# Kernel tuning notes

Hardware: AMD Instinct MI355X
Metric: run time of the kernel (lower is better)

## Reference

```python
import jax, jax.numpy as jnp
import numpy as np

B, P = 4, 65536
TD, HID, OUT = 32, 128, 4
RES = 256
NFREQ = 6
CD = 3 * 2 * NFREQ  # frequency encoding out dim


def setup_inputs() -> dict:
    key = jax.random.key(0)
    ks = jax.random.split(key, 12)

    def w(k, shape):
        fan_in = shape[-1]
        return jax.random.normal(k, shape, jnp.float32) / np.sqrt(fan_in)

    return {
        "triplane": jax.random.normal(ks[0], (3 * B, TD, RES, RES), jnp.float32),
        "coords": jax.random.uniform(ks[1], (B, P, 3), jnp.float32),  # inside aabb [-1,1]^3
        "w_in": w(ks[2], (HID, TD + CD)),
        "b_in": jnp.zeros((HID,), jnp.float32),
        "w_skip": w(ks[3], (HID, TD + CD)),
        "b_skip": jnp.zeros((HID,), jnp.float32),
        "w_before": w(ks[4], (2, HID, HID)),
        "b_before": jnp.zeros((2, HID), jnp.float32),
        "w_after": w(ks[5], (2, HID, HID)),
        "b_after": jnp.zeros((2, HID), jnp.float32),
        "w_out": w(ks[6], (OUT, HID)),
        "b_out": jnp.zeros((OUT,), jnp.float32),
    }


@jax.custom_vjp
def trunc_exp(x):
    return jnp.exp(x)


def _trunc_exp_fwd(x):
    return jnp.exp(x), x


def _trunc_exp_bwd(x, g):
    return (g * jnp.exp(jnp.clip(x, -15.0, 15.0)),)


trunc_exp.defvjp(_trunc_exp_fwd, _trunc_exp_bwd)


def grid_sample_bilinear(feat, gx, gy):
    # feat: [N, C, H, W]; gx, gy: [N, Q] in [-1, 1]; align_corners=True, zero padding.
    N, C, H, W = feat.shape
    ix = (gx + 1.0) * 0.5 * (W - 1)
    iy = (gy + 1.0) * 0.5 * (H - 1)
    x0 = jnp.floor(ix)
    y0 = jnp.floor(iy)
    wx1 = ix - x0
    wy1 = iy - y0
    feat_flat = feat.reshape(N, C, H * W)

    def gather(xf, yf):
        xi = xf.astype(jnp.int32)
        yi = yf.astype(jnp.int32)
        valid = ((xi >= 0) & (xi < W) & (yi >= 0) & (yi < H)).astype(feat.dtype)
        xi = jnp.clip(xi, 0, W - 1)
        yi = jnp.clip(yi, 0, H - 1)
        idx = yi * W + xi  # [N, Q]
        g = jnp.take_along_axis(feat_flat, idx[:, None, :], axis=2)  # [N, C, Q]
        return g * valid[:, None, :]

    out = (
        gather(x0, y0) * ((1 - wx1) * (1 - wy1))[:, None, :]
        + gather(x0 + 1, y0) * (wx1 * (1 - wy1))[:, None, :]
        + gather(x0, y0 + 1) * ((1 - wx1) * wy1)[:, None, :]
        + gather(x0 + 1, y0 + 1) * (wx1 * wy1)[:, None, :]
    )
    return out  # [N, C, Q]


def freq_encode(x):
    # x: [B, P, 3] in [0, 1]; NeRF-style frequency encoding (tcnn 'Frequency').
    freqs = (2.0 ** jnp.arange(NFREQ, dtype=x.dtype)) * jnp.pi  # [NFREQ]
    ang = x[..., :, None] * freqs  # [B, P, 3, NFREQ]
    enc = jnp.concatenate([jnp.sin(ang), jnp.cos(ang)], axis=-1)  # [B, P, 3, 2*NFREQ]
    return enc.reshape(x.shape[0], x.shape[1], CD)


def reference(triplane, coords, w_in, b_in, w_skip, b_skip, w_before, b_before,
              w_after, b_after, w_out, b_out):
    aabb_min = jnp.full((3,), -1.0, jnp.float32)
    aabb_max = jnp.full((3,), 1.0, jnp.float32)

    scaled = 2.0 * (coords - aabb_min) / (aabb_max - aabb_min) - 1.0  # [-1,1]
    norm = (coords - aabb_min) / (aabb_max - aabb_min)  # [0,1]
    selector = jnp.all((norm > 0.0) & (norm < 1.0), axis=-1)  # [B, P]

    # planes: xy=(x,y), xz=(x,z), zy=(y,z); stacked per batch -> [3B, P, 2]
    coords_xy = scaled[:, :, (0, 1)]
    coords_xz = scaled[:, :, (0, 2)]
    coords_zy = scaled[:, :, (1, 2)]
    grid = jnp.stack([coords_xy, coords_xz, coords_zy], axis=1).reshape(3 * B, P, 2)

    feats = grid_sample_bilinear(triplane, grid[..., 0], grid[..., 1])  # [3B, TD, P]
    feats = feats.transpose(0, 2, 1).reshape(B, 3, P, TD).sum(axis=1)  # [B, P, TD]

    h = jnp.concatenate([freq_encode(norm), feats], axis=-1)  # [B, P, CD+TD]

    lin = lambda x, w, b: jnp.einsum("bpf,hf->bph", x, w) + b
    x = jax.nn.relu(lin(h, w_in, b_in))
    for i in range(w_before.shape[0]):
        x = jax.nn.relu(lin(x, w_before[i], b_before[i]))
    x = x + jax.nn.relu(lin(h, w_skip, b_skip))
    for i in range(w_after.shape[0]):
        x = jax.nn.relu(lin(x, w_after[i], b_after[i]))
    x = lin(x, w_out, b_out)  # [B, P, 4]

    rgb = jax.nn.sigmoid(x[..., :3])
    density = trunc_exp(x[..., 3:4] - 1.0) * selector[..., None].astype(x.dtype)
    return rgb, density
```

## Files before the change

kernel.cpp:

```cpp
#include <hip/hip_runtime.h>
#include <stdint.h>

typedef short short8 __attribute__((ext_vector_type(8)));
typedef float floatx16 __attribute__((ext_vector_type(16)));
typedef unsigned int uint32;

#define NPTS (4 * 65536)
#define RGB_OFF (NPTS * 3)

__device__ __forceinline__ uint16_t bf_rne(float f) {
  uint32 u = __float_as_uint(f);
  u += 0x7FFFu + ((u >> 16) & 1u);
  return (uint16_t)(u >> 16);
}
__device__ __forceinline__ uint32 pack2(float a, float b) {
  uint32 ua = (__float_as_uint(a) + 0x8000u) >> 16;
  uint32 ub = (__float_as_uint(b) + 0x8000u) & 0xFFFF0000u;
  return ua | ub;
}
__device__ __forceinline__ void gacc(const uint16_t* p, float w, float* acc) {
  uint4 q = *(const uint4*)p;
  acc[0] += w * __uint_as_float(q.x << 16);
  acc[1] += w * __uint_as_float(q.x & 0xFFFF0000u);
  acc[2] += w * __uint_as_float(q.y << 16);
  acc[3] += w * __uint_as_float(q.y & 0xFFFF0000u);
  acc[4] += w * __uint_as_float(q.z << 16);
  acc[5] += w * __uint_as_float(q.z & 0xFFFF0000u);
  acc[6] += w * __uint_as_float(q.w << 16);
  acc[7] += w * __uint_as_float(q.w & 0xFFFF0000u);
}

__global__ __launch_bounds__(256) void k_tr(const float* __restrict__ tri,
                                            uint16_t* __restrict__ out) {
  __shared__ uint16_t tile[32 * 258];
  const int blk = blockIdx.x;
  const int n = blk >> 8, y = blk & 255;
  const int t = threadIdx.x;
  for (int c = 0; c < 32; ++c) {
    float v = tri[((size_t)(n * 32 + c)) * 65536 + y * 256 + t];
    tile[c * 258 + t] = bf_rne(v);
  }
  __syncthreads();
  uint16_t* dst = out + ((size_t)(n * 256 + y)) * 256 * 32;
  const int c0 = (t & 7) * 4;
  for (int i = 0; i < 8; ++i) {
    int x = (t >> 3) + 32 * i;
    uint32 d0 = (uint32)tile[(c0 + 0) * 258 + x] | ((uint32)tile[(c0 + 1) * 258 + x] << 16);
    uint32 d1 = (uint32)tile[(c0 + 2) * 258 + x] | ((uint32)tile[(c0 + 3) * 258 + x] << 16);
    *(uint2*)(dst + x * 32 + c0) = make_uint2(d0, d1);
  }
}

__global__ __launch_bounds__(256) void k_pack(
    const float* __restrict__ w_in, const float* __restrict__ w_skip,
    const float* __restrict__ w_before, const float* __restrict__ w_after,
    const float* __restrict__ w_out, const float* __restrict__ b_in,
    const float* __restrict__ b_skip, const float* __restrict__ b_before,
    const float* __restrict__ b_after, const float* __restrict__ b_out,
    uint16_t* __restrict__ wpack, float* __restrict__ bpack) {
  const int blk = blockIdx.x;
  if (blk >= 44) {
    for (int t = threadIdx.x; t < 800; t += 256) {
      int l, idx;
      if (t < 768) { l = t >> 7; idx = t & 127; }
      else { l = 6; idx = t - 768; }
      int mt = idx >> 5, rem = idx & 31;
      int half = rem >> 4, r = rem & 15;
      int f = mt * 32 + (r & 3) + 8 * (r >> 2) + 4 * half;
      float v;
      switch (l) {
        case 0: v = b_in[f]; break;
        case 1: v = b_before[f]; break;
        case 2: v = b_before[128 + f]; break;
        case 3: v = b_skip[f]; break;
        case 4: v = b_after[f]; break;
        case 5: v = b_after[128 + f]; break;
        default: v = (f < 4) ? b_out[f] : 0.0f; break;
      }
      bpack[l * 128 + idx] = v;
    }
    return;
  }
  const int w = blk * 4 + (threadIdx.x >> 6);
  const int L = threadIdx.x & 63;
  int lay, mt, k;
  if (w < 20)      { lay = 0; mt = w / 5;        k = w - mt * 5; }
  else if (w < 52) { int u = w - 20;  lay = 1; mt = u >> 3; k = u & 7; }
  else if (w < 84) { int u = w - 52;  lay = 2; mt = u >> 3; k = u & 7; }
  else if (w < 104){ int u = w - 84;  lay = 3; mt = u / 5;  k = u - mt * 5; }
  else if (w < 136){ int u = w - 104; lay = 4; mt = u >> 3; k = u & 7; }
  else if (w < 168){ int u = w - 136; lay = 5; mt = u >> 3; k = u & 7; }
  else             { lay = 6; mt = 0; k = w - 168; }
  const float* W;
  int insk = 0;
  switch (lay) {
    case 0: W = w_in; insk = 1; break;
    case 1: W = w_before; break;
    case 2: W = w_before + 16384; break;
    case 3: W = w_skip; insk = 1; break;
    case 4: W = w_after; break;
    case 5: W = w_after + 16384; break;
    default: W = w_out; break;
  }
  const int frow = mt * 32 + (L & 31);
  const int kbase = k * 16 + (L >> 5) * 8;
  uint16_t h[8];
#pragma unroll
  for (int j = 0; j < 8; ++j) {
    int kl = kbase + j;
    float v;
    if (insk) {
      int col = (kl < 32) ? (36 + kl) : ((kl < 68) ? (kl - 32) : -1);
      v = (col < 0) ? 0.0f : W[frow * 68 + col];
    } else if (lay == 6) {
      v = (frow < 4) ? W[frow * 128 + kl] : 0.0f;
    } else {
      v = W[frow * 128 + kl];
    }
    h[j] = bf_rne(v);
  }
  uint4 q;
  q.x = (uint32)h[0] | ((uint32)h[1] << 16);
  q.y = (uint32)h[2] | ((uint32)h[3] << 16);
  q.z = (uint32)h[4] | ((uint32)h[5] << 16);
  q.w = (uint32)h[6] | ((uint32)h[7] << 16);
  *(uint4*)(wpack + (size_t)w * 512 + L * 8) = q;
}

template <int LAY, int Ks, int FOFF, bool FROMH, bool SKIP>
__device__ __forceinline__ void mlp_layer(const uint16_t* __restrict__ hrow,
                                          uint16_t* __restrict__ arow,
                                          const uint16_t* __restrict__ wpack,
                                          const float* __restrict__ bpack,
                                          int ih, int kh, int L, int ps) {
  const uint16_t* src = FROMH ? hrow : (const uint16_t*)arow;
  short8 bfr[Ks];
#pragma unroll
  for (int k = 0; k < Ks; ++k)
    bfr[k] = *(const short8*)(src + (((2 * k + kh) ^ ps) << 3));
  if (!FROMH) __syncthreads();
#pragma unroll
  for (int m = 0; m < 2; ++m) {
    const int mt = ih * 2 + m;
    const float4* bp = (const float4*)(bpack + LAY * 128 + mt * 32 + kh * 16);
    float4 b0 = bp[0], b1 = bp[1], b2 = bp[2], b3 = bp[3];
    floatx16 acc;
    acc[0] = b0.x; acc[1] = b0.y; acc[2] = b0.z; acc[3] = b0.w;
    acc[4] = b1.x; acc[5] = b1.y; acc[6] = b1.z; acc[7] = b1.w;
    acc[8] = b2.x; acc[9] = b2.y; acc[10] = b2.z; acc[11] = b2.w;
    acc[12] = b3.x; acc[13] = b3.y; acc[14] = b3.z; acc[15] = b3.w;
    const uint16_t* wp = wpack + (size_t)(FOFF + mt * Ks) * 512 + L * 8;
#pragma unroll
    for (int k = 0; k < Ks; ++k) {
      short8 af = *(const short8*)(wp + k * 512);
      acc = __builtin_amdgcn_mfma_f32_32x32x16_bf16(af, bfr[k], acc, 0, 0, 0);
    }
#pragma unroll
    for (int g = 0; g < 4; ++g) {
      float v0 = fmaxf(acc[4 * g + 0], 0.f), v1 = fmaxf(acc[4 * g + 1], 0.f);
      float v2 = fmaxf(acc[4 * g + 2], 0.f), v3 = fmaxf(acc[4 * g + 3], 0.f);
      const int byte = 64 * mt + 16 * g + 8 * kh;
      uint16_t* dst =
          (uint16_t*)((char*)arow + ((((byte >> 4)) ^ ps) << 4) + (byte & 15));
      if (SKIP) {
        uint2 old = *(const uint2*)dst;
        v0 += __uint_as_float(old.x << 16);
        v1 += __uint_as_float(old.x & 0xFFFF0000u);
        v2 += __uint_as_float(old.y << 16);
        v3 += __uint_as_float(old.y & 0xFFFF0000u);
      }
      *(uint2*)dst = make_uint2(pack2(v0, v1), pack2(v2, v3));
    }
  }
  __syncthreads();
}

__global__ __launch_bounds__(256, 2) void k_main(
    const uint16_t* __restrict__ trit, const float* __restrict__ trif,
    const float* __restrict__ coords, const uint16_t* __restrict__ wpack,
    const float* __restrict__ bpack, float* __restrict__ dout, int fast) {
  __shared__ __align__(16) uint16_t h_s[64 * 128];
  __shared__ __align__(16) uint16_t a_s[64 * 128];
  const int t = threadIdx.x;

  {
    const int p = t >> 2, c = t & 3;
    const int pg = blockIdx.x * 64 + p;
    float cx = coords[pg * 3 + 0], cy = coords[pg * 3 + 1], cz = coords[pg * 3 + 2];
    float f1x = cx + 1.0f, f1y = cy + 1.0f, f1z = cz + 1.0f;
    float nx = f1x * 0.5f, ny = f1y * 0.5f, nz = f1z * 0.5f;
    float sx = f1x - 1.0f, sy = f1y - 1.0f, sz = f1z - 1.0f;
    bool sel = (nx > 0.f) & (nx < 1.f) & (ny > 0.f) & (ny < 1.f) & (nz > 0.f) & (nz < 1.f);
    const int b = pg >> 16;
    float acc[8];
#pragma unroll
    for (int j = 0; j < 8; ++j) acc[j] = 0.f;
#pragma unroll
    for (int pl = 0; pl < 3; ++pl) {
      float gx = (pl == 2) ? sy : sx;
      float gy = (pl == 0) ? sy : sz;
      float ix = ((gx + 1.0f) * 0.5f) * 255.0f;
      float iy = ((gy + 1.0f) * 0.5f) * 255.0f;
      float x0f = floorf(ix), y0f = floorf(iy);
      float wx = ix - x0f, wy = iy - y0f;
      float vx0 = (x0f >= 0.0f && x0f < 256.0f) ? 1.f : 0.f;
      float vx1 = (x0f >= -1.0f && x0f < 255.0f) ? 1.f : 0.f;
      float vy0 = (y0f >= 0.0f && y0f < 256.0f) ? 1.f : 0.f;
      float vy1 = (y0f >= -1.0f && y0f < 255.0f) ? 1.f : 0.f;
      int x0 = min(max((int)x0f, 0), 255), x1 = min(max((int)x0f + 1, 0), 255);
      int y0 = min(max((int)y0f, 0), 255), y1 = min(max((int)y0f + 1, 0), 255);
      float w00 = (1.f - wx) * (1.f - wy) * vx0 * vy0;
      float w10 = wx * (1.f - wy) * vx1 * vy0;
      float w01 = (1.f - wx) * wy * vx0 * vy1;
      float w11 = wx * wy * vx1 * vy1;
      const int n = 3 * b + pl;
      if (fast) {
        const uint16_t* base = trit + ((size_t)n << 21) + (c << 3);
        gacc(base + ((size_t)(y0 * 256 + x0) << 5), w00, acc);
        gacc(base + ((size_t)(y0 * 256 + x1) << 5), w10, acc);
        gacc(base + ((size_t)(y1 * 256 + x0) << 5), w01, acc);
        gacc(base + ((size_t)(y1 * 256 + x1) << 5), w11, acc);
      } else {
        const float* basef = trif + ((size_t)(n * 32 + c * 8) << 16);
#pragma unroll
        for (int jj = 0; jj < 8; ++jj) {
          const float* chp = basef + ((size_t)jj << 16);
          acc[jj] += w00 * chp[y0 * 256 + x0] + w10 * chp[y0 * 256 + x1] +
                     w01 * chp[y1 * 256 + x0] + w11 * chp[y1 * 256 + x1];
        }
      }
    }
    const int s = p & 15;
    uint16_t* hrow = h_s + p * 128;
    *(uint4*)(hrow + (((c ^ s)) << 3)) =
        make_uint4(pack2(acc[0], acc[1]), pack2(acc[2], acc[3]),
                   pack2(acc[4], acc[5]), pack2(acc[6], acc[7]));
    if (c < 3) {
      float nd = (c == 0) ? nx : (c == 1) ? ny : nz;
      float vals[12];
#pragma unroll
      for (int k = 0; k < 6; ++k) {
        float rev = nd * (0.5f * (float)(1 << k));
        float r = rev - rintf(rev);
        vals[k] = __builtin_amdgcn_sinf(r);
        vals[6 + k] = __builtin_amdgcn_cosf(r);
      }
#pragma unroll
      for (int iw = 0; iw < 3; ++iw) {
        int byte = 64 + 24 * c + 8 * iw;
        int chunk = byte >> 4, off = byte & 15;
        *(uint2*)((char*)hrow + (((chunk ^ s)) << 4) + off) =
            make_uint2(pack2(vals[4 * iw + 0], vals[4 * iw + 1]),
                       pack2(vals[4 * iw + 2], vals[4 * iw + 3]));
      }
    } else {
      *(uint2*)((char*)hrow + (((8 ^ s)) << 4) + 8) = make_uint2(0u, 0u);
      uint32 selw = sel ? 0x3F800000u : 0u;
      *(uint4*)((char*)hrow + (((9 ^ s)) << 4)) = make_uint4(0u, 0u, 0u, selw);
    }
  }
  __syncthreads();

  const int w = t >> 6, L = t & 63;
  const int ih = w & 1, jh = w >> 1;
  const int kh = L >> 5;
  const int prow = jh * 32 + (L & 31);
  const int ps = prow & 15;
  const uint16_t* hrow = h_s + prow * 128;
  uint16_t* arow = a_s + prow * 128;

  mlp_layer<0, 5, 0,   true,  false>(hrow, arow, wpack, bpack, ih, kh, L, ps);
  mlp_layer<1, 8, 20,  false, false>(hrow, arow, wpack, bpack, ih, kh, L, ps);
  mlp_layer<2, 8, 52,  false, false>(hrow, arow, wpack, bpack, ih, kh, L, ps);
  mlp_layer<3, 5, 84,  true,  true >(hrow, arow, wpack, bpack, ih, kh, L, ps);
  mlp_layer<4, 8, 104, false, false>(hrow, arow, wpack, bpack, ih, kh, L, ps);
  mlp_layer<5, 8, 136, false, false>(hrow, arow, wpack, bpack, ih, kh, L, ps);

  if (ih == 0) {
    short8 bfr[8];
#pragma unroll
    for (int k = 0; k < 8; ++k)
      bfr[k] = *(const short8*)(arow + (((2 * k + kh) ^ ps) << 3));
    const float4* bp = (const float4*)(bpack + 768 + kh * 16);
    float4 b0 = bp[0], b1 = bp[1], b2 = bp[2], b3 = bp[3];
    floatx16 acc;
    acc[0] = b0.x; acc[1] = b0.y; acc[2] = b0.z; acc[3] = b0.w;
    acc[4] = b1.x; acc[5] = b1.y; acc[6] = b1.z; acc[7] = b1.w;
    acc[8] = b2.x; acc[9] = b2.y; acc[10] = b2.z; acc[11] = b2.w;
    acc[12] = b3.x; acc[13] = b3.y; acc[14] = b3.z; acc[15] = b3.w;
    const uint16_t* wp = wpack + (size_t)168 * 512 + L * 8;
#pragma unroll
    for (int k = 0; k < 8; ++k) {
      short8 af = *(const short8*)(wp + k * 512);
      acc = __builtin_amdgcn_mfma_f32_32x32x16_bf16(af, bfr[k], acc, 0, 0, 0);
    }
    if (kh == 0) {
      const int pg = blockIdx.x * 64 + prow;
      const float l2e = 1.44269504f;
      float r0 = 1.0f / (1.0f + exp2f(-l2e * acc[0]));
      float r1 = 1.0f / (1.0f + exp2f(-l2e * acc[1]));
      float r2 = 1.0f / (1.0f + exp2f(-l2e * acc[2]));
      uint16_t sv = hrow[(((9 ^ ps)) << 3) + 7];
      float dens = exp2f((acc[3] - 1.0f) * l2e) * (sv ? 1.0f : 0.0f);
      dout[pg * 3 + 0] = r0;
      dout[pg * 3 + 1] = r1;
      dout[pg * 3 + 2] = r2;
      dout[RGB_OFF + pg] = dens;
    }
  }
}

extern "C" void kernel_launch(void* const* d_in, const int* in_sizes, int n_in,
                              void* d_out, int out_size, void* d_ws, size_t ws_size,
                              hipStream_t stream) {
  const float* tri = (const float*)d_in[0];
  const float* coords = (const float*)d_in[1];
  const float* w_in = (const float*)d_in[2];
  const float* b_in = (const float*)d_in[3];
  const float* w_skip = (const float*)d_in[4];
  const float* b_skip = (const float*)d_in[5];
  const float* w_bef = (const float*)d_in[6];
  const float* b_bef = (const float*)d_in[7];
  const float* w_aft = (const float*)d_in[8];
  const float* b_aft = (const float*)d_in[9];
  const float* w_out = (const float*)d_in[10];
  const float* b_out = (const float*)d_in[11];
  const size_t TRI_B = (size_t)12 * 256 * 256 * 32 * 2;
  const size_t WP_B = (size_t)176 * 1024;
  const size_t BP_B = 3200;
  char* ws = (char*)d_ws;
  const int fast = (ws_size >= TRI_B + WP_B + BP_B) ? 1 : 0;
  uint16_t* trit;
  uint16_t* wpk;
  float* bpk;
  if (fast) {
    trit = (uint16_t*)ws;
    wpk = (uint16_t*)(ws + TRI_B);
    bpk = (float*)(ws + TRI_B + WP_B);
  } else {
    trit = (uint16_t*)ws;
    wpk = (uint16_t*)ws;
    bpk = (float*)(ws + WP_B);
  }
  if (fast) k_tr<<<dim3(3072), dim3(256), 0, stream>>>(tri, trit);
  k_pack<<<dim3(45), dim3(256), 0, stream>>>(w_in, w_skip, w_bef, w_aft, w_out,
                                             b_in, b_skip, b_bef, b_aft, b_out,
                                             wpk, bpk);
  k_main<<<dim3(4096), dim3(256), 0, stream>>>(trit, tri, coords, wpk, bpk,
                                               (float*)d_out, fast);
}
```

Measured before the change: 295.2 us.

## Process 128 points per block with 2x2 MFMA register tiling per wave

Each block now handles 128 points instead of 64, and each wave computes a 2x2 tile of 32x32 MFMA outputs, so every weight fragment loaded from global memory feeds two point tiles and is fetched half as often per point. The gather phase gives each thread two 16-byte chunks of features and reorganizes the frequency-encoding writes as full 16-byte stores. pack2 now uses a single byte-permute instruction. The grid is halved and shared memory doubles to 64KB per block, which together with higher register use may reduce occupancy below the two blocks per CU requested.

```diff
diff --git a/kernel.cpp b/kernel.cpp
--- a/kernel.cpp
+++ b/kernel.cpp
@@ -14,9 +14,8 @@
   return (uint16_t)(u >> 16);
 }
 __device__ __forceinline__ uint32 pack2(float a, float b) {
-  uint32 ua = (__float_as_uint(a) + 0x8000u) >> 16;
-  uint32 ub = (__float_as_uint(b) + 0x8000u) & 0xFFFF0000u;
-  return ua | ub;
+  return __builtin_amdgcn_perm(__float_as_uint(b) + 0x8000u,
+                               __float_as_uint(a) + 0x8000u, 0x07060302u);
 }
 __device__ __forceinline__ void gacc(const uint16_t* p, float w, float* acc) {
   uint4 q = *(const uint4*)p;
@@ -128,48 +127,66 @@
 }
 
 template <int LAY, int Ks, int FOFF, bool FROMH, bool SKIP>
-__device__ __forceinline__ void mlp_layer(const uint16_t* __restrict__ hrow,
-                                          uint16_t* __restrict__ arow,
-                                          const uint16_t* __restrict__ wpack,
-                                          const float* __restrict__ bpack,
-                                          int ih, int kh, int L, int ps) {
-  const uint16_t* src = FROMH ? hrow : (const uint16_t*)arow;
-  short8 bfr[Ks];
-#pragma unroll
-  for (int k = 0; k < Ks; ++k)
-    bfr[k] = *(const short8*)(src + (((2 * k + kh) ^ ps) << 3));
+__device__ __forceinline__ void mlp_layer(
+    const uint16_t* __restrict__ hrow0, const uint16_t* __restrict__ hrow1,
+    uint16_t* __restrict__ arow0, uint16_t* __restrict__ arow1,
+    const uint16_t* __restrict__ wpack, const float* __restrict__ bpack,
+    int mt0, int kh, int L, int ps) {
+  const uint16_t* src0 = FROMH ? hrow0 : (const uint16_t*)arow0;
+  const uint16_t* src1 = FROMH ? hrow1 : (const uint16_t*)arow1;
+  short8 b0[Ks], b1[Ks];
+#pragma unroll
+  for (int k = 0; k < Ks; ++k) {
+    b0[k] = *(const short8*)(src0 + (((2 * k + kh) ^ ps) << 3));
+    b1[k] = *(const short8*)(src1 + (((2 * k + kh) ^ ps) << 3));
+  }
   if (!FROMH) __syncthreads();
-#pragma unroll
-  for (int m = 0; m < 2; ++m) {
-    const int mt = ih * 2 + m;
-    const float4* bp = (const float4*)(bpack + LAY * 128 + mt * 32 + kh * 16);
-    float4 b0 = bp[0], b1 = bp[1], b2 = bp[2], b3 = bp[3];
-    floatx16 acc;
-    acc[0] = b0.x; acc[1] = b0.y; acc[2] = b0.z; acc[3] = b0.w;
-    acc[4] = b1.x; acc[5] = b1.y; acc[6] = b1.z; acc[7] = b1.w;
-    acc[8] = b2.x; acc[9] = b2.y; acc[10] = b2.z; acc[11] = b2.w;
-    acc[12] = b3.x; acc[13] = b3.y; acc[14] = b3.z; acc[15] = b3.w;
-    const uint16_t* wp = wpack + (size_t)(FOFF + mt * Ks) * 512 + L * 8;
-#pragma unroll
-    for (int k = 0; k < Ks; ++k) {
-      short8 af = *(const short8*)(wp + k * 512);
-      acc = __builtin_amdgcn_mfma_f32_32x32x16_bf16(af, bfr[k], acc, 0, 0, 0);
-    }
+  floatx16 a00, a01, a10, a11;
+  {
+    const float4* bp0 = (const float4*)(bpack + LAY * 128 + mt0 * 32 + kh * 16);
+    const float4* bp1 = (const float4*)(bpack + LAY * 128 + (mt0 + 1) * 32 + kh * 16);
 #pragma unroll
     for (int g = 0; g < 4; ++g) {
-      float v0 = fmaxf(acc[4 * g + 0], 0.f), v1 = fmaxf(acc[4 * g + 1], 0.f);
-      float v2 = fmaxf(acc[4 * g + 2], 0.f), v3 = fmaxf(acc[4 * g + 3], 0.f);
-      const int byte = 64 * mt + 16 * g + 8 * kh;
-      uint16_t* dst =
-          (uint16_t*)((char*)arow + ((((byte >> 4)) ^ ps) << 4) + (byte & 15));
-      if (SKIP) {
-        uint2 old = *(const uint2*)dst;
-        v0 += __uint_as_float(old.x << 16);
-        v1 += __uint_as_float(old.x & 0xFFFF0000u);
-        v2 += __uint_as_float(old.y << 16);
-        v3 += __uint_as_float(old.y & 0xFFFF0000u);
-      }
-      *(uint2*)dst = make_uint2(pack2(v0, v1), pack2(v2, v3));
+      float4 v0 = bp0[g], v1 = bp1[g];
+      a00[4 * g + 0] = v0.x; a00[4 * g + 1] = v0.y; a00[4 * g + 2] = v0.z; a00[4 * g + 3] = v0.w;
+      a10[4 * g + 0] = v1.x; a10[4 * g + 1] = v1.y; a10[4 * g + 2] = v1.z; a10[4 * g + 3] = v1.w;
+    }
+    a01 = a00; a11 = a10;
+  }
+  const uint16_t* wp0 = wpack + (size_t)(FOFF + mt0 * Ks) * 512 + L * 8;
+  const uint16_t* wp1 = wp0 + (size_t)Ks * 512;
+#pragma unroll
+  for (int k = 0; k < Ks; ++k) {
+    short8 af0 = *(const short8*)(wp0 + k * 512);
+    short8 af1 = *(const short8*)(wp1 + k * 512);
+    a00 = __builtin_amdgcn_mfma_f32_32x32x16_bf16(af0, b0[k], a00, 0, 0, 0);
+    a01 = __builtin_amdgcn_mfma_f32_32x32x16_bf16(af0, b1[k], a01, 0, 0, 0);
+    a10 = __builtin_amdgcn_mfma_f32_32x32x16_bf16(af1, b0[k], a10, 0, 0, 0);
+    a11 = __builtin_amdgcn_mfma_f32_32x32x16_bf16(af1, b1[k], a11, 0, 0, 0);
+  }
+#pragma unroll
+  for (int mi = 0; mi < 2; ++mi) {
+    const int mt = mt0 + mi;
+#pragma unroll
+    for (int j = 0; j < 2; ++j) {
+      uint16_t* arow = j ? arow1 : arow0;
+      const floatx16& ac = mi ? (j ? a11 : a10) : (j ? a01 : a00);
+#pragma unroll
+      for (int g = 0; g < 4; ++g) {
+        float v0 = fmaxf(ac[4 * g + 0], 0.f), v1 = fmaxf(ac[4 * g + 1], 0.f);
+        float v2 = fmaxf(ac[4 * g + 2], 0.f), v3 = fmaxf(ac[4 * g + 3], 0.f);
+        const int byte = 64 * mt + 16 * g + 8 * kh;
+        uint16_t* dst =
+            (uint16_t*)((char*)arow + ((((byte >> 4)) ^ ps) << 4) + (byte & 15));
+        if (SKIP) {
+          uint2 old = *(const uint2*)dst;
+          v0 += __uint_as_float(old.x << 16);
+          v1 += __uint_as_float(old.x & 0xFFFF0000u);
+          v2 += __uint_as_float(old.y << 16);
+          v3 += __uint_as_float(old.y & 0xFFFF0000u);
+        }
+        *(uint2*)dst = make_uint2(pack2(v0, v1), pack2(v2, v3));
+      }
     }
   }
   __syncthreads();
@@ -179,22 +196,22 @@
     const uint16_t* __restrict__ trit, const float* __restrict__ trif,
     const float* __restrict__ coords, const uint16_t* __restrict__ wpack,
     const float* __restrict__ bpack, float* __restrict__ dout, int fast) {
-  __shared__ __align__(16) uint16_t h_s[64 * 128];
-  __shared__ __align__(16) uint16_t a_s[64 * 128];
+  __shared__ __align__(16) uint16_t h_s[128 * 128];
+  __shared__ __align__(16) uint16_t a_s[128 * 128];
   const int t = threadIdx.x;
 
   {
-    const int p = t >> 2, c = t & 3;
-    const int pg = blockIdx.x * 64 + p;
+    const int p = t >> 1, c = t & 1;
+    const int pg = blockIdx.x * 128 + p;
     float cx = coords[pg * 3 + 0], cy = coords[pg * 3 + 1], cz = coords[pg * 3 + 2];
     float f1x = cx + 1.0f, f1y = cy + 1.0f, f1z = cz + 1.0f;
     float nx = f1x * 0.5f, ny = f1y * 0.5f, nz = f1z * 0.5f;
     float sx = f1x - 1.0f, sy = f1y - 1.0f, sz = f1z - 1.0f;
     bool sel = (nx > 0.f) & (nx < 1.f) & (ny > 0.f) & (ny < 1.f) & (nz > 0.f) & (nz < 1.f);
     const int b = pg >> 16;
-    float acc[8];
-#pragma unroll
-    for (int j = 0; j < 8; ++j) acc[j] = 0.f;
+    float acc[16];
+#pragma unroll
+    for (int j = 0; j < 16; ++j) acc[j] = 0.f;
 #pragma unroll
     for (int pl = 0; pl < 3; ++pl) {
       float gx = (pl == 2) ? sy : sx;
@@ -215,15 +232,19 @@
       float w11 = wx * wy * vx1 * vy1;
       const int n = 3 * b + pl;
       if (fast) {
-        const uint16_t* base = trit + ((size_t)n << 21) + (c << 3);
-        gacc(base + ((size_t)(y0 * 256 + x0) << 5), w00, acc);
-        gacc(base + ((size_t)(y0 * 256 + x1) << 5), w10, acc);
-        gacc(base + ((size_t)(y1 * 256 + x0) << 5), w01, acc);
-        gacc(base + ((size_t)(y1 * 256 + x1) << 5), w11, acc);
+        const uint16_t* base = trit + ((size_t)n << 21) + (c << 4);
+        const uint16_t* p00 = base + ((size_t)(y0 * 256 + x0) << 5);
+        const uint16_t* p10 = base + ((size_t)(y0 * 256 + x1) << 5);
+        const uint16_t* p01 = base + ((size_t)(y1 * 256 + x0) << 5);
+        const uint16_t* p11 = base + ((size_t)(y1 * 256 + x1) << 5);
+        gacc(p00, w00, acc); gacc(p00 + 8, w00, acc + 8);
+        gacc(p10, w10, acc); gacc(p10 + 8, w10, acc + 8);
+        gacc(p01, w01, acc); gacc(p01 + 8, w01, acc + 8);
+        gacc(p11, w11, acc); gacc(p11 + 8, w11, acc + 8);
       } else {
-        const float* basef = trif + ((size_t)(n * 32 + c * 8) << 16);
-#pragma unroll
-        for (int jj = 0; jj < 8; ++jj) {
+        const float* basef = trif + ((size_t)(n * 32 + c * 16) << 16);
+#pragma unroll
+        for (int jj = 0; jj < 16; ++jj) {
           const float* chp = basef + ((size_t)jj << 16);
           acc[jj] += w00 * chp[y0 * 256 + x0] + w10 * chp[y0 * 256 + x1] +
                      w01 * chp[y1 * 256 + x0] + w11 * chp[y1 * 256 + x1];
@@ -232,80 +253,111 @@
     }
     const int s = p & 15;
     uint16_t* hrow = h_s + p * 128;
-    *(uint4*)(hrow + (((c ^ s)) << 3)) =
+    *(uint4*)(hrow + (((2 * c + 0) ^ s) << 3)) =
         make_uint4(pack2(acc[0], acc[1]), pack2(acc[2], acc[3]),
                    pack2(acc[4], acc[5]), pack2(acc[6], acc[7]));
-    if (c < 3) {
-      float nd = (c == 0) ? nx : (c == 1) ? ny : nz;
-      float vals[12];
+    *(uint4*)(hrow + (((2 * c + 1) ^ s) << 3)) =
+        make_uint4(pack2(acc[8], acc[9]), pack2(acc[10], acc[11]),
+                   pack2(acc[12], acc[13]), pack2(acc[14], acc[15]));
+    if (c == 0) {
+      float v[24];
+#pragma unroll
+      for (int d = 0; d < 2; ++d) {
+        float nd = d ? ny : nx;
+#pragma unroll
+        for (int k = 0; k < 6; ++k) {
+          float rev = nd * (0.5f * (float)(1 << k));
+          float r = rev - rintf(rev);
+          v[12 * d + k] = __builtin_amdgcn_sinf(r);
+          v[12 * d + 6 + k] = __builtin_amdgcn_cosf(r);
+        }
+      }
+      *(uint4*)(hrow + ((4 ^ s) << 3)) =
+          make_uint4(pack2(v[0], v[1]), pack2(v[2], v[3]), pack2(v[4], v[5]), pack2(v[6], v[7]));
+      *(uint4*)(hrow + ((5 ^ s) << 3)) =
+          make_uint4(pack2(v[8], v[9]), pack2(v[10], v[11]), pack2(v[12], v[13]), pack2(v[14], v[15]));
+      *(uint4*)(hrow + ((6 ^ s) << 3)) =
+          make_uint4(pack2(v[16], v[17]), pack2(v[18], v[19]), pack2(v[20], v[21]), pack2(v[22], v[23]));
+    } else {
+      float v[12];
 #pragma unroll
       for (int k = 0; k < 6; ++k) {
-        float rev = nd * (0.5f * (float)(1 << k));
+        float rev = nz * (0.5f * (float)(1 << k));
         float r = rev - rintf(rev);
-        vals[k] = __builtin_amdgcn_sinf(r);
-        vals[6 + k] = __builtin_amdgcn_cosf(r);
-      }
-#pragma unroll
-      for (int iw = 0; iw < 3; ++iw) {
-        int byte = 64 + 24 * c + 8 * iw;
-        int chunk = byte >> 4, off = byte & 15;
-        *(uint2*)((char*)hrow + (((chunk ^ s)) << 4) + off) =
-            make_uint2(pack2(vals[4 * iw + 0], vals[4 * iw + 1]),
-                       pack2(vals[4 * iw + 2], vals[4 * iw + 3]));
-      }
-    } else {
-      *(uint2*)((char*)hrow + (((8 ^ s)) << 4) + 8) = make_uint2(0u, 0u);
+        v[k] = __builtin_amdgcn_sinf(r);
+        v[6 + k] = __builtin_amdgcn_cosf(r);
+      }
+      *(uint4*)(hrow + ((7 ^ s) << 3)) =
+          make_uint4(pack2(v[0], v[1]), pack2(v[2], v[3]), pack2(v[4], v[5]), pack2(v[6], v[7]));
+      *(uint4*)(hrow + ((8 ^ s) << 3)) =
+          make_uint4(pack2(v[8], v[9]), pack2(v[10], v[11]), 0u, 0u);
       uint32 selw = sel ? 0x3F800000u : 0u;
-      *(uint4*)((char*)hrow + (((9 ^ s)) << 4)) = make_uint4(0u, 0u, 0u, selw);
+      *(uint4*)(hrow + ((9 ^ s) << 3)) = make_uint4(0u, 0u, 0u, selw);
     }
   }
   __syncthreads();
 
   const int w = t >> 6, L = t & 63;
-  const int ih = w & 1, jh = w >> 1;
+  const int mt0 = (w & 1) * 2;
+  const int jq = w >> 1;
   const int kh = L >> 5;
-  const int prow = jh * 32 + (L & 31);
-  const int ps = prow & 15;
-  const uint16_t* hrow = h_s + prow * 128;
-  uint16_t* arow = a_s + prow * 128;
-
-  mlp_layer<0, 5, 0,   true,  false>(hrow, arow, wpack, bpack, ih, kh, L, ps);
-  mlp_layer<1, 8, 20,  false, false>(hrow, arow, wpack, bpack, ih, kh, L, ps);
-  mlp_layer<2, 8, 52,  false, false>(hrow, arow, wpack, bpack, ih, kh, L, ps);
-  mlp_layer<3, 5, 84,  true,  true >(hrow, arow, wpack, bpack, ih, kh, L, ps);
-  mlp_layer<4, 8, 104, false, false>(hrow, arow, wpack, bpack, ih, kh, L, ps);
-  mlp_layer<5, 8, 136, false, false>(hrow, arow, wpack, bpack, ih, kh, L, ps);
-
-  if (ih == 0) {
-    short8 bfr[8];
-#pragma unroll
-    for (int k = 0; k < 8; ++k)
-      bfr[k] = *(const short8*)(arow + (((2 * k + kh) ^ ps) << 3));
-    const float4* bp = (const float4*)(bpack + 768 + kh * 16);
-    float4 b0 = bp[0], b1 = bp[1], b2 = bp[2], b3 = bp[3];
-    floatx16 acc;
-    acc[0] = b0.x; acc[1] = b0.y; acc[2] = b0.z; acc[3] = b0.w;
-    acc[4] = b1.x; acc[5] = b1.y; acc[6] = b1.z; acc[7] = b1.w;
-    acc[8] = b2.x; acc[9] = b2.y; acc[10] = b2.z; acc[11] = b2.w;
-    acc[12] = b3.x; acc[13] = b3.y; acc[14] = b3.z; acc[15] = b3.w;
+  const int prow0 = jq * 64 + (L & 31);
+  const int prow1 = prow0 + 32;
+  const int ps = prow0 & 15;
+  const uint16_t* hrow0 = h_s + prow0 * 128;
+  const uint16_t* hrow1 = h_s + prow1 * 128;
+  uint16_t* arow0 = a_s + prow0 * 128;
+  uint16_t* arow1 = a_s + prow1 * 128;
+
+  mlp_layer<0, 5, 0,   true,  false>(hrow0, hrow1, arow0, arow1, wpack, bpack, mt0, kh, L, ps);
+  mlp_layer<1, 8, 20,  false, false>(hrow0, hrow1, arow0, arow1, wpack, bpack, mt0, kh, L, ps);
+  mlp_layer<2, 8, 52,  false, false>(hrow0, hrow1, arow0, arow1, wpack, bpack, mt0, kh, L, ps);
+  mlp_layer<3, 5, 84,  true,  true >(hrow0, hrow1, arow0, arow1, wpack, bpack, mt0, kh, L, ps);
+  mlp_layer<4, 8, 104, false, false>(hrow0, hrow1, arow0, arow1, wpack, bpack, mt0, kh, L, ps);
+  mlp_layer<5, 8, 136, false, false>(hrow0, hrow1, arow0, arow1, wpack, bpack, mt0, kh, L, ps);
+
+  if (mt0 == 0) {
+    short8 b0[8], b1[8];
+#pragma unroll
+    for (int k = 0; k < 8; ++k) {
+      b0[k] = *(const short8*)(arow0 + (((2 * k + kh) ^ ps) << 3));
+      b1[k] = *(const short8*)(arow1 + (((2 * k + kh) ^ ps) << 3));
+    }
+    floatx16 a0, a1;
+    {
+      const float4* bp = (const float4*)(bpack + 768 + kh * 16);
+#pragma unroll
+      for (int g = 0; g < 4; ++g) {
+        float4 v = bp[g];
+        a0[4 * g + 0] = v.x; a0[4 * g + 1] = v.y; a0[4 * g + 2] = v.z; a0[4 * g + 3] = v.w;
+      }
+      a1 = a0;
+    }
     const uint16_t* wp = wpack + (size_t)168 * 512 + L * 8;
 #pragma unroll
     for (int k = 0; k < 8; ++k) {
       short8 af = *(const short8*)(wp + k * 512);
-      acc = __builtin_amdgcn_mfma_f32_32x32x16_bf16(af, bfr[k], acc, 0, 0, 0);
+      a0 = __builtin_amdgcn_mfma_f32_32x32x16_bf16(af, b0[k], a0, 0, 0, 0);
+      a1 = __builtin_amdgcn_mfma_f32_32x32x16_bf16(af, b1[k], a1, 0, 0, 0);
     }
     if (kh == 0) {
-      const int pg = blockIdx.x * 64 + prow;
       const float l2e = 1.44269504f;
-      float r0 = 1.0f / (1.0f + exp2f(-l2e * acc[0]));
-      float r1 = 1.0f / (1.0f + exp2f(-l2e * acc[1]));
-      float r2 = 1.0f / (1.0f + exp2f(-l2e * acc[2]));
-      uint16_t sv = hrow[(((9 ^ ps)) << 3) + 7];
-      float dens = exp2f((acc[3] - 1.0f) * l2e) * (sv ? 1.0f : 0.0f);
-      dout[pg * 3 + 0] = r0;
-      dout[pg * 3 + 1] = r1;
-      dout[pg * 3 + 2] = r2;
-      dout[RGB_OFF + pg] = dens;
+#pragma unroll
+      for (int j = 0; j < 2; ++j) {
+        const floatx16& ac = j ? a1 : a0;
+        const int prow = j ? prow1 : prow0;
+        const uint16_t* hrow = j ? hrow1 : hrow0;
+        const int pg = blockIdx.x * 128 + prow;
+        float r0 = 1.0f / (1.0f + exp2f(-l2e * ac[0]));
+        float r1 = 1.0f / (1.0f + exp2f(-l2e * ac[1]));
+        float r2 = 1.0f / (1.0f + exp2f(-l2e * ac[2]));
+        uint16_t sv = hrow[((9 ^ ps) << 3) + 7];
+        float dens = exp2f((ac[3] - 1.0f) * l2e) * (sv ? 1.0f : 0.0f);
+        dout[pg * 3 + 0] = r0;
+        dout[pg * 3 + 1] = r1;
+        dout[pg * 3 + 2] = r2;
+        dout[RGB_OFF + pg] = dens;
+      }
     }
   }
 }
@@ -346,6 +398,6 @@
   k_pack<<<dim3(45), dim3(256), 0, stream>>>(w_in, w_skip, w_bef, w_aft, w_out,
                                              b_in, b_skip, b_bef, b_aft, b_out,
                                              wpk, bpk);
-  k_main<<<dim3(4096), dim3(256), 0, stream>>>(trit, tri, coords, wpk, bpk,
+  k_main<<<dim3(2048), dim3(256), 0, stream>>>(trit, tri, coords, wpk, bpk,
                                                (float*)d_out, fast);
 }
```

Result: faster. 278.4 us (-5.7%).

## Keep MLP activations in registers via permlane swaps instead of LDS round-trips

Applied to the files above, without the earlier changes.

Removes the shared-memory staging of features and per-layer activations. Each wave now owns 32 points and computes all four 32-row output tiles itself, and MFMA outputs are converted into the next layer's B-operand layout in registers with v_permlane32_swap. The per-layer __syncthreads and LDS traffic go away, blocks grow to 128 points, and the occupancy hint is raised to 3. The cost is more registers per thread (four accumulators plus 8 short8 operands), which may cause spills, and each wave now loads the full weight set.

```diff
diff --git a/kernel.cpp b/kernel.cpp
--- a/kernel.cpp
+++ b/kernel.cpp
@@ -14,20 +14,24 @@
   return (uint16_t)(u >> 16);
 }
 __device__ __forceinline__ uint32 pack2(float a, float b) {
-  uint32 ua = (__float_as_uint(a) + 0x8000u) >> 16;
-  uint32 ub = (__float_as_uint(b) + 0x8000u) & 0xFFFF0000u;
-  return ua | ub;
+  return __builtin_amdgcn_perm(__float_as_uint(b) + 0x8000u,
+                               __float_as_uint(a) + 0x8000u, 0x07060302u);
+}
+__device__ __forceinline__ float bf_lo(uint32 u) { return __uint_as_float(u << 16); }
+__device__ __forceinline__ float bf_hi(uint32 u) { return __uint_as_float(u & 0xFFFF0000u); }
+__device__ __forceinline__ void swap32(uint32& a, uint32& b) {
+  asm("v_permlane32_swap_b32 %0, %1" : "+v"(a), "+v"(b));
 }
 __device__ __forceinline__ void gacc(const uint16_t* p, float w, float* acc) {
   uint4 q = *(const uint4*)p;
-  acc[0] += w * __uint_as_float(q.x << 16);
-  acc[1] += w * __uint_as_float(q.x & 0xFFFF0000u);
-  acc[2] += w * __uint_as_float(q.y << 16);
-  acc[3] += w * __uint_as_float(q.y & 0xFFFF0000u);
-  acc[4] += w * __uint_as_float(q.z << 16);
-  acc[5] += w * __uint_as_float(q.z & 0xFFFF0000u);
-  acc[6] += w * __uint_as_float(q.w << 16);
-  acc[7] += w * __uint_as_float(q.w & 0xFFFF0000u);
+  acc[0] += w * bf_lo(q.x);
+  acc[1] += w * bf_hi(q.x);
+  acc[2] += w * bf_lo(q.y);
+  acc[3] += w * bf_hi(q.y);
+  acc[4] += w * bf_lo(q.z);
+  acc[5] += w * bf_hi(q.z);
+  acc[6] += w * bf_lo(q.w);
+  acc[7] += w * bf_hi(q.w);
 }
 
 __global__ __launch_bounds__(256) void k_tr(const float* __restrict__ tri,
@@ -127,181 +131,213 @@
   *(uint4*)(wpack + (size_t)w * 512 + L * 8) = q;
 }
 
-template <int LAY, int Ks, int FOFF, bool FROMH, bool SKIP>
-__device__ __forceinline__ void mlp_layer(const uint16_t* __restrict__ hrow,
-                                          uint16_t* __restrict__ arow,
-                                          const uint16_t* __restrict__ wpack,
-                                          const float* __restrict__ bpack,
-                                          int ih, int kh, int L, int ps) {
-  const uint16_t* src = FROMH ? hrow : (const uint16_t*)arow;
-  short8 bfr[Ks];
-#pragma unroll
-  for (int k = 0; k < Ks; ++k)
-    bfr[k] = *(const short8*)(src + (((2 * k + kh) ^ ps) << 3));
-  if (!FROMH) __syncthreads();
-#pragma unroll
-  for (int m = 0; m < 2; ++m) {
-    const int mt = ih * 2 + m;
+
+template <int LAY, int Ks, int FOFF>
+__device__ __forceinline__ void mfma_block(floatx16* a, const short8* bin,
+                                           const uint16_t* __restrict__ wpack,
+                                           const float* __restrict__ bpack, int L,
+                                           int kh) {
+#pragma unroll
+  for (int mt = 0; mt < 4; ++mt) {
     const float4* bp = (const float4*)(bpack + LAY * 128 + mt * 32 + kh * 16);
-    float4 b0 = bp[0], b1 = bp[1], b2 = bp[2], b3 = bp[3];
-    floatx16 acc;
-    acc[0] = b0.x; acc[1] = b0.y; acc[2] = b0.z; acc[3] = b0.w;
-    acc[4] = b1.x; acc[5] = b1.y; acc[6] = b1.z; acc[7] = b1.w;
-    acc[8] = b2.x; acc[9] = b2.y; acc[10] = b2.z; acc[11] = b2.w;
-    acc[12] = b3.x; acc[13] = b3.y; acc[14] = b3.z; acc[15] = b3.w;
-    const uint16_t* wp = wpack + (size_t)(FOFF + mt * Ks) * 512 + L * 8;
-#pragma unroll
-    for (int k = 0; k < Ks; ++k) {
-      short8 af = *(const short8*)(wp + k * 512);
-      acc = __builtin_amdgcn_mfma_f32_32x32x16_bf16(af, bfr[k], acc, 0, 0, 0);
-    }
 #pragma unroll
     for (int g = 0; g < 4; ++g) {
-      float v0 = fmaxf(acc[4 * g + 0], 0.f), v1 = fmaxf(acc[4 * g + 1], 0.f);
-      float v2 = fmaxf(acc[4 * g + 2], 0.f), v3 = fmaxf(acc[4 * g + 3], 0.f);
-      const int byte = 64 * mt + 16 * g + 8 * kh;
-      uint16_t* dst =
-          (uint16_t*)((char*)arow + ((((byte >> 4)) ^ ps) << 4) + (byte & 15));
-      if (SKIP) {
-        uint2 old = *(const uint2*)dst;
-        v0 += __uint_as_float(old.x << 16);
-        v1 += __uint_as_float(old.x & 0xFFFF0000u);
-        v2 += __uint_as_float(old.y << 16);
-        v3 += __uint_as_float(old.y & 0xFFFF0000u);
-      }
-      *(uint2*)dst = make_uint2(pack2(v0, v1), pack2(v2, v3));
-    }
-  }
-  __syncthreads();
-}
-
-__global__ __launch_bounds__(256, 2) void k_main(
+      float4 v = bp[g];
+      a[mt][4 * g + 0] = v.x; a[mt][4 * g + 1] = v.y;
+      a[mt][4 * g + 2] = v.z; a[mt][4 * g + 3] = v.w;
+    }
+  }
+  const uint16_t* wp = wpack + (size_t)FOFF * 512 + L * 8;
+#pragma unroll
+  for (int k = 0; k < Ks; ++k) {
+    short8 w0 = *(const short8*)(wp + (size_t)(0 * Ks + k) * 512);
+    short8 w1 = *(const short8*)(wp + (size_t)(1 * Ks + k) * 512);
+    short8 w2 = *(const short8*)(wp + (size_t)(2 * Ks + k) * 512);
+    short8 w3 = *(const short8*)(wp + (size_t)(3 * Ks + k) * 512);
+    a[0] = __builtin_amdgcn_mfma_f32_32x32x16_bf16(w0, bin[k], a[0], 0, 0, 0);
+    a[1] = __builtin_amdgcn_mfma_f32_32x32x16_bf16(w1, bin[k], a[1], 0, 0, 0);
+    a[2] = __builtin_amdgcn_mfma_f32_32x32x16_bf16(w2, bin[k], a[2], 0, 0, 0);
+    a[3] = __builtin_amdgcn_mfma_f32_32x32x16_bf16(w3, bin[k], a[3], 0, 0, 0);
+  }
+}
+
+template <int LAY, int Ks, int FOFF>
+__device__ __forceinline__ void layer_dense(const short8* bin, short8* bout,
+                                            const uint16_t* __restrict__ wpack,
+                                            const float* __restrict__ bpack, int L,
+                                            int kh) {
+  floatx16 a[4];
+  mfma_block<LAY, Ks, FOFF>(a, bin, wpack, bpack, L, kh);
+#pragma unroll
+  for (int f = 0; f < 8; ++f) {
+    const int mt = f >> 1, s = f & 1;
+    uint32 q0a = pack2(fmaxf(a[mt][8 * s + 0], 0.f), fmaxf(a[mt][8 * s + 1], 0.f));
+    uint32 q0b = pack2(fmaxf(a[mt][8 * s + 2], 0.f), fmaxf(a[mt][8 * s + 3], 0.f));
+    uint32 q1a = pack2(fmaxf(a[mt][8 * s + 4], 0.f), fmaxf(a[mt][8 * s + 5], 0.f));
+    uint32 q1b = pack2(fmaxf(a[mt][8 * s + 6], 0.f), fmaxf(a[mt][8 * s + 7], 0.f));
+    swap32(q0a, q1a);
+    swap32(q0b, q1b);
+    bout[f] = __builtin_bit_cast(short8, make_uint4(q0a, q0b, q1a, q1b));
+  }
+}
+
+template <int LAY, int Ks, int FOFF>
+__device__ __forceinline__ void layer_skip(const short8* hin, short8* bio,
+                                           const uint16_t* __restrict__ wpack,
+                                           const float* __restrict__ bpack, int L,
+                                           int kh) {
+  floatx16 a[4];
+  mfma_block<LAY, Ks, FOFF>(a, hin, wpack, bpack, L, kh);
+#pragma unroll
+  for (int f = 0; f < 8; ++f) {
+    const int mt = f >> 1, s = f & 1;
+    uint4 old = __builtin_bit_cast(uint4, bio[f]);
+    uint32 uA = old.x, uB = old.y, uC = old.z, uD = old.w;
+    swap32(uA, uC);
+    swap32(uB, uD);
+    float r0 = fmaxf(a[mt][8 * s + 0], 0.f) + bf_lo(uA);
+    float r1 = fmaxf(a[mt][8 * s + 1], 0.f) + bf_hi(uA);
+    float r2 = fmaxf(a[mt][8 * s + 2], 0.f) + bf_lo(uB);
+    float r3 = fmaxf(a[mt][8 * s + 3], 0.f) + bf_hi(uB);
+    float r4 = fmaxf(a[mt][8 * s + 4], 0.f) + bf_lo(uC);
+    float r5 = fmaxf(a[mt][8 * s + 5], 0.f) + bf_hi(uC);
+    float r6 = fmaxf(a[mt][8 * s + 6], 0.f) + bf_lo(uD);
+    float r7 = fmaxf(a[mt][8 * s + 7], 0.f) + bf_hi(uD);
+    uint32 q0a = pack2(r0, r1), q0b = pack2(r2, r3);
+    uint32 q1a = pack2(r4, r5), q1b = pack2(r6, r7);
+    swap32(q0a, q1a);
+    swap32(q0b, q1b);
+    bio[f] = __builtin_bit_cast(short8, make_uint4(q0a, q0b, q1a, q1b));
+  }
+}
+
+__global__ __launch_bounds__(256, 3) void k_main(
     const uint16_t* __restrict__ trit, const float* __restrict__ trif,
     const float* __restrict__ coords, const uint16_t* __restrict__ wpack,
     const float* __restrict__ bpack, float* __restrict__ dout, int fast) {
-  __shared__ __align__(16) uint16_t h_s[64 * 128];
-  __shared__ __align__(16) uint16_t a_s[64 * 128];
   const int t = threadIdx.x;
-
+  const int L = t & 63;
+  const int kh = L >> 5;
+  const int p = (t >> 6) * 32 + (L & 31);
+  const int pg = blockIdx.x * 128 + p;
+
+  float cx = coords[pg * 3 + 0], cy = coords[pg * 3 + 1], cz = coords[pg * 3 + 2];
+  float f1x = cx + 1.0f, f1y = cy + 1.0f, f1z = cz + 1.0f;
+  float nx = f1x * 0.5f, ny = f1y * 0.5f, nz = f1z * 0.5f;
+  float sx = f1x - 1.0f, sy = f1y - 1.0f, sz = f1z - 1.0f;
+  bool sel = (nx > 0.f) & (nx < 1.f) & (ny > 0.f) & (ny < 1.f) & (nz > 0.f) & (nz < 1.f);
+  const int b = pg >> 16;
+  float acc[16];
+#pragma unroll
+  for (int j = 0; j < 16; ++j) acc[j] = 0.f;
+#pragma unroll
+  for (int pl = 0; pl < 3; ++pl) {
+    float gx = (pl == 2) ? sy : sx;
+    float gy = (pl == 0) ? sy : sz;
+    float ix = ((gx + 1.0f) * 0.5f) * 255.0f;
+    float iy = ((gy + 1.0f) * 0.5f) * 255.0f;
+    float x0f = floorf(ix), y0f = floorf(iy);
+    float wx = ix - x0f, wy = iy - y0f;
+    float vx0 = (x0f >= 0.0f && x0f < 256.0f) ? 1.f : 0.f;
+    float vx1 = (x0f >= -1.0f && x0f < 255.0f) ? 1.f : 0.f;
+    float vy0 = (y0f >= 0.0f && y0f < 256.0f) ? 1.f : 0.f;
+    float vy1 = (y0f >= -1.0f && y0f < 255.0f) ? 1.f : 0.f;
+    int x0 = min(max((int)x0f, 0), 255), x1 = min(max((int)x0f + 1, 0), 255);
+    int y0 = min(max((int)y0f, 0), 255), y1 = min(max((int)y0f + 1, 0), 255);
+    float w00 = (1.f - wx) * (1.f - wy) * vx0 * vy0;
+    float w10 = wx * (1.f - wy) * vx1 * vy0;
+    float w01 = (1.f - wx) * wy * vx0 * vy1;
+    float w11 = wx * wy * vx1 * vy1;
+    const int n = 3 * b + pl;
+    if (fast) {
+      const uint16_t* cb = trit + ((size_t)n << 21) + kh * 8;
+      size_t o00 = (size_t)(y0 * 256 + x0) << 5, o10 = (size_t)(y0 * 256 + x1) << 5;
+      size_t o01 = (size_t)(y1 * 256 + x0) << 5, o11 = (size_t)(y1 * 256 + x1) << 5;
+      gacc(cb + o00, w00, acc); gacc(cb + 16 + o00, w00, acc + 8);
+      gacc(cb + o10, w10, acc); gacc(cb + 16 + o10, w10, acc + 8);
+      gacc(cb + o01, w01, acc); gacc(cb + 16 + o01, w01, acc + 8);
+      gacc(cb + o11, w11, acc); gacc(cb + 16 + o11, w11, acc + 8);
+    } else {
+      const float* basef = trif + (((size_t)n * 32) << 16);
+#pragma unroll
+      for (int j = 0; j < 8; ++j) {
+        const float* c0p = basef + (((size_t)(kh * 8 + j)) << 16);
+        const float* c1p = basef + (((size_t)(16 + kh * 8 + j)) << 16);
+        acc[j] += w00 * c0p[y0 * 256 + x0] + w10 * c0p[y0 * 256 + x1] +
+                  w01 * c0p[y1 * 256 + x0] + w11 * c0p[y1 * 256 + x1];
+        acc[8 + j] += w00 * c1p[y0 * 256 + x0] + w10 * c1p[y0 * 256 + x1] +
+                      w01 * c1p[y1 * 256 + x0] + w11 * c1p[y1 * 256 + x1];
+      }
+    }
+  }
+  short8 hf[5];
+  hf[0] = __builtin_bit_cast(
+      short8, make_uint4(pack2(acc[0], acc[1]), pack2(acc[2], acc[3]),
+                         pack2(acc[4], acc[5]), pack2(acc[6], acc[7])));
+  hf[1] = __builtin_bit_cast(
+      short8, make_uint4(pack2(acc[8], acc[9]), pack2(acc[10], acc[11]),
+                         pack2(acc[12], acc[13]), pack2(acc[14], acc[15])));
   {
-    const int p = t >> 2, c = t & 3;
-    const int pg = blockIdx.x * 64 + p;
-    float cx = coords[pg * 3 + 0], cy = coords[pg * 3 + 1], cz = coords[pg * 3 + 2];
-    float f1x = cx + 1.0f, f1y = cy + 1.0f, f1z = cz + 1.0f;
-    float nx = f1x * 0.5f, ny = f1y * 0.5f, nz = f1z * 0.5f;
-    float sx = f1x - 1.0f, sy = f1y - 1.0f, sz = f1z - 1.0f;
-    bool sel = (nx > 0.f) & (nx < 1.f) & (ny > 0.f) & (ny < 1.f) & (nz > 0.f) & (nz < 1.f);
-    const int b = pg >> 16;
-    float acc[8];
-#pragma unroll
-    for (int j = 0; j < 8; ++j) acc[j] = 0.f;
-#pragma unroll
-    for (int pl = 0; pl < 3; ++pl) {
-      float gx = (pl == 2) ? sy : sx;
-      float gy = (pl == 0) ? sy : sz;
-      float ix = ((gx + 1.0f) * 0.5f) * 255.0f;
-      float iy = ((gy + 1.0f) * 0.5f) * 255.0f;
-      float x0f = floorf(ix), y0f = floorf(iy);
-      float wx = ix - x0f, wy = iy - y0f;
-      float vx0 = (x0f >= 0.0f && x0f < 256.0f) ? 1.f : 0.f;
-      float vx1 = (x0f >= -1.0f && x0f < 255.0f) ? 1.f : 0.f;
-      float vy0 = (y0f >= 0.0f && y0f < 256.0f) ? 1.f : 0.f;
-      float vy1 = (y0f >= -1.0f && y0f < 255.0f) ? 1.f : 0.f;
-      int x0 = min(max((int)x0f, 0), 255), x1 = min(max((int)x0f + 1, 0), 255);
-      int y0 = min(max((int)y0f, 0), 255), y1 = min(max((int)y0f + 1, 0), 255);
-      float w00 = (1.f - wx) * (1.f - wy) * vx0 * vy0;
-      float w10 = wx * (1.f - wy) * vx1 * vy0;
-      float w01 = (1.f - wx) * wy * vx0 * vy1;
-      float w11 = wx * wy * vx1 * vy1;
-      const int n = 3 * b + pl;
-      if (fast) {
-        const uint16_t* base = trit + ((size_t)n << 21) + (c << 3);
-        gacc(base + ((size_t)(y0 * 256 + x0) << 5), w00, acc);
-        gacc(base + ((size_t)(y0 * 256 + x1) << 5), w10, acc);
-        gacc(base + ((size_t)(y1 * 256 + x0) << 5), w01, acc);
-        gacc(base + ((size_t)(y1 * 256 + x1) << 5), w11, acc);
-      } else {
-        const float* basef = trif + ((size_t)(n * 32 + c * 8) << 16);
-#pragma unroll
-        for (int jj = 0; jj < 8; ++jj) {
-          const float* chp = basef + ((size_t)jj << 16);
-          acc[jj] += w00 * chp[y0 * 256 + x0] + w10 * chp[y0 * 256 + x1] +
-                     w01 * chp[y1 * 256 + x0] + w11 * chp[y1 * 256 + x1];
-        }
-      }
-    }
-    const int s = p & 15;
-    uint16_t* hrow = h_s + p * 128;
-    *(uint4*)(hrow + (((c ^ s)) << 3)) =
-        make_uint4(pack2(acc[0], acc[1]), pack2(acc[2], acc[3]),
-                   pack2(acc[4], acc[5]), pack2(acc[6], acc[7]));
-    if (c < 3) {
-      float nd = (c == 0) ? nx : (c == 1) ? ny : nz;
-      float vals[12];
+    float sv[3][6], cv[3][6];
+#pragma unroll
+    for (int d = 0; d < 3; ++d) {
+      float nd = (d == 0) ? nx : (d == 1) ? ny : nz;
 #pragma unroll
       for (int k = 0; k < 6; ++k) {
         float rev = nd * (0.5f * (float)(1 << k));
         float r = rev - rintf(rev);
-        vals[k] = __builtin_amdgcn_sinf(r);
-        vals[6 + k] = __builtin_amdgcn_cosf(r);
+        sv[d][k] = __builtin_amdgcn_sinf(r);
+        cv[d][k] = __builtin_amdgcn_cosf(r);
       }
-#pragma unroll
-      for (int iw = 0; iw < 3; ++iw) {
-        int byte = 64 + 24 * c + 8 * iw;
-        int chunk = byte >> 4, off = byte & 15;
-        *(uint2*)((char*)hrow + (((chunk ^ s)) << 4) + off) =
-            make_uint2(pack2(vals[4 * iw + 0], vals[4 * iw + 1]),
-                       pack2(vals[4 * iw + 2], vals[4 * iw + 3]));
-      }
+    }
+    if (kh == 0) {
+      hf[2] = __builtin_bit_cast(
+          short8, make_uint4(pack2(sv[0][0], sv[0][1]), pack2(sv[0][2], sv[0][3]),
+                             pack2(sv[0][4], sv[0][5]), pack2(cv[0][0], cv[0][1])));
+      hf[3] = __builtin_bit_cast(
+          short8, make_uint4(pack2(sv[1][4], sv[1][5]), pack2(cv[1][0], cv[1][1]),
+                             pack2(cv[1][2], cv[1][3]), pack2(cv[1][4], cv[1][5])));
+      hf[4] = __builtin_bit_cast(
+          short8, make_uint4(pack2(cv[2][2], cv[2][3]), pack2(cv[2][4], cv[2][5]), 0u, 0u));
     } else {
-      *(uint2*)((char*)hrow + (((8 ^ s)) << 4) + 8) = make_uint2(0u, 0u);
-      uint32 selw = sel ? 0x3F800000u : 0u;
-      *(uint4*)((char*)hrow + (((9 ^ s)) << 4)) = make_uint4(0u, 0u, 0u, selw);
-    }
-  }
-  __syncthreads();
-
-  const int w = t >> 6, L = t & 63;
-  const int ih = w & 1, jh = w >> 1;
-  const int kh = L >> 5;
-  const int prow = jh * 32 + (L & 31);
-  const int ps = prow & 15;
-  const uint16_t* hrow = h_s + prow * 128;
-  uint16_t* arow = a_s + prow * 128;
-
-  mlp_layer<0, 5, 0,   true,  false>(hrow, arow, wpack, bpack, ih, kh, L, ps);
-  mlp_layer<1, 8, 20,  false, false>(hrow, arow, wpack, bpack, ih, kh, L, ps);
-  mlp_layer<2, 8, 52,  false, false>(hrow, arow, wpack, bpack, ih, kh, L, ps);
-  mlp_layer<3, 5, 84,  true,  true >(hrow, arow, wpack, bpack, ih, kh, L, ps);
-  mlp_layer<4, 8, 104, false, false>(hrow, arow, wpack, bpack, ih, kh, L, ps);
-  mlp_layer<5, 8, 136, false, false>(hrow, arow, wpack, bpack, ih, kh, L, ps);
-
-  if (ih == 0) {
-    short8 bfr[8];
-#pragma unroll
-    for (int k = 0; k < 8; ++k)
-      bfr[k] = *(const short8*)(arow + (((2 * k + kh) ^ ps) << 3));
+      hf[2] = __builtin_bit_cast(
+          short8, make_uint4(pack2(cv[0][2], cv[0][3]), pack2(cv[0][4], cv[0][5]),
+                             pack2(sv[1][0], sv[1][1]), pack2(sv[1][2], sv[1][3])));
+      hf[3] = __builtin_bit_cast(
+          short8, make_uint4(pack2(sv[2][0], sv[2][1]), pack2(sv[2][2], sv[2][3]),
+                             pack2(sv[2][4], sv[2][5]), pack2(cv[2][0], cv[2][1])));
+      hf[4] = __builtin_bit_cast(short8, make_uint4(0u, 0u, 0u, 0u));
+    }
+  }
+
+  short8 bf[8];
+  layer_dense<0, 5, 0>(hf, bf, wpack, bpack, L, kh);
+  layer_dense<1, 8, 20>(bf, bf, wpack, bpack, L, kh);
+  layer_dense<2, 8, 52>(bf, bf, wpack, bpack, L, kh);
+  layer_skip<3, 5, 84>(hf, bf, wpack, bpack, L, kh);
+  layer_dense<4, 8, 104>(bf, bf, wpack, bpack, L, kh);
+  layer_dense<5, 8, 136>(bf, bf, wpack, bpack, L, kh);
+
+  {
+    floatx16 a;
     const float4* bp = (const float4*)(bpack + 768 + kh * 16);
-    float4 b0 = bp[0], b1 = bp[1], b2 = bp[2], b3 = bp[3];
-    floatx16 acc;
-    acc[0] = b0.x; acc[1] = b0.y; acc[2] = b0.z; acc[3] = b0.w;
-    acc[4] = b1.x; acc[5] = b1.y; acc[6] = b1.z; acc[7] = b1.w;
-    acc[8] = b2.x; acc[9] = b2.y; acc[10] = b2.z; acc[11] = b2.w;
-    acc[12] = b3.x; acc[13] = b3.y; acc[14] = b3.z; acc[15] = b3.w;
+#pragma unroll
+    for (int g = 0; g < 4; ++g) {
+      float4 v = bp[g];
+      a[4 * g + 0] = v.x; a[4 * g + 1] = v.y; a[4 * g + 2] = v.z; a[4 * g + 3] = v.w;
+    }
     const uint16_t* wp = wpack + (size_t)168 * 512 + L * 8;
 #pragma unroll
     for (int k = 0; k < 8; ++k) {
-      short8 af = *(const short8*)(wp + k * 512);
-      acc = __builtin_amdgcn_mfma_f32_32x32x16_bf16(af, bfr[k], acc, 0, 0, 0);
+      short8 af = *(const short8*)(wp + (size_t)k * 512);
+      a = __builtin_amdgcn_mfma_f32_32x32x16_bf16(af, bf[k], a, 0, 0, 0);
     }
     if (kh == 0) {
-      const int pg = blockIdx.x * 64 + prow;
       const float l2e = 1.44269504f;
-      float r0 = 1.0f / (1.0f + exp2f(-l2e * acc[0]));
-      float r1 = 1.0f / (1.0f + exp2f(-l2e * acc[1]));
-      float r2 = 1.0f / (1.0f + exp2f(-l2e * acc[2]));
-      uint16_t sv = hrow[(((9 ^ ps)) << 3) + 7];
-      float dens = exp2f((acc[3] - 1.0f) * l2e) * (sv ? 1.0f : 0.0f);
+      float r0 = 1.0f / (1.0f + exp2f(-l2e * a[0]));
+      float r1 = 1.0f / (1.0f + exp2f(-l2e * a[1]));
+      float r2 = 1.0f / (1.0f + exp2f(-l2e * a[2]));
+      float dens = exp2f((a[3] - 1.0f) * l2e) * (sel ? 1.0f : 0.0f);
       dout[pg * 3 + 0] = r0;
       dout[pg * 3 + 1] = r1;
       dout[pg * 3 + 2] = r2;
@@ -346,6 +382,6 @@
   k_pack<<<dim3(45), dim3(256), 0, stream>>>(w_in, w_skip, w_bef, w_aft, w_out,
                                              b_in, b_skip, b_bef, b_aft, b_out,
                                              wpk, bpk);
-  k_main<<<dim3(4096), dim3(256), 0, stream>>>(trit, tri, coords, wpk, bpk,
+  k_main<<<dim3(2048), dim3(256), 0, stream>>>(trit, tri, coords, wpk, bpk,
                                                (float*)d_out, fast);
 }
```

Result: faster. 272.2 us (-7.8%).
